# Optimization experiments

Hardware: AMD Instinct MI355X
Metric: run time of the kernel (lower is better)

## Reference

```python
import jax, jax.numpy as jnp
import numpy as np

BETA = 0.9      # LIF leak
THRESH = 1.0    # snntorch Leaky default threshold
SLOPE = 25.0    # fast_sigmoid surrogate slope

@jax.custom_vjp
def spike(x):
    # Heaviside forward, fast_sigmoid surrogate backward
    return (x > 0).astype(x.dtype)

def _spike_fwd(x):
    return spike(x), x

def _spike_bwd(x, g):
    return (g / (SLOPE * jnp.abs(x) + 1.0) ** 2,)

spike.defvjp(_spike_fwd, _spike_bwd)


def setup_inputs() -> dict:
    key = jax.random.key(0)
    k0, k1, k2, k3, k4 = jax.random.split(key, 5)
    B, T, I, H, C = 256, 100, 512, 1024, 8
    x = jax.random.normal(k0, (B, T, I), dtype=jnp.float32)
    s1 = 1.0 / np.sqrt(I)
    s2 = 1.0 / np.sqrt(H)
    W1 = jax.random.uniform(k1, (H, I), jnp.float32, -s1, s1)
    b1 = jax.random.uniform(k2, (H,), jnp.float32, -s1, s1)
    W2 = jax.random.uniform(k3, (C, H), jnp.float32, -s2, s2)
    b2 = jax.random.uniform(k4, (C,), jnp.float32, -s2, s2)
    return {"x": x, "W1": W1, "b1": b1, "W2": W2, "b2": b2}


def reference(x, W1, b1, W2, b2):
    # x: [B, T, I]
    B, T, I = x.shape
    H = W1.shape[0]
    # fc1 for all timesteps as one big GEMM (same math as per-step loop).
    cur = jnp.einsum('bti,hi->tbh', x, W1) + b1  # [T, B, H]

    def step(mem, c):
        # snntorch Leaky (reset_mechanism='subtract'):
        reset = spike(mem - THRESH)
        mem_new = BETA * mem + c - reset * THRESH
        spk = spike(mem_new - THRESH)
        return mem_new, spk

    mem0 = jnp.zeros((B, H), dtype=x.dtype)
    _, spk_rec = jax.lax.scan(step, mem0, cur)  # spk_rec: [T, B, H]

    # sum_t (spk_t @ W2.T + b2) == (sum_t spk_t) @ W2.T + T*b2
    spk_sum = spk_rec.sum(axis=0)  # [B, H]
    logits = spk_sum @ W2.T + T * b2  # [B, C]
    return logits
```

## Files before the change

kernel.cpp:

```cpp
#include <hip/hip_runtime.h>


#define B_   256
#define T_   100
#define I_   512
#define H_   1024
#define C_   8
#define M_   (B_ * T_)
#define SC   64.0f
#define ISC  (1.0f / 4096.0f)

#define CELL_  512
#define SHALF_ 16384
#define PANEL_ 32768

typedef _Float16 half8 __attribute__((ext_vector_type(8)));
typedef float floatx16 __attribute__((ext_vector_type(16)));

__device__ __forceinline__ void ld_g2l(const _Float16* g, _Float16* l) {
    __builtin_amdgcn_global_load_lds(
        (const __attribute__((address_space(1))) void*)g,
        (__attribute__((address_space(3))) void*)l, 16, 0, 0);
}

__global__ void __launch_bounds__(256)
split_all(const float* __restrict__ x, const float* __restrict__ W1,
          const float* __restrict__ b2, _Float16* __restrict__ Asp,
          float* __restrict__ out) {
    const int tid = threadIdx.x;
    const int lane = tid & 63;
    const int w = tid >> 6;
    const int p = blockIdx.x;
    int g = p * 256 + tid;
    if (g < B_ * C_) out[g] = 100.0f * b2[g & (C_ - 1)];

    const bool isA = (p < 800);
    const int pl = isA ? p : (p - 800);
    const float* srcm = isA ? x : W1;
    _Float16* dstp = Asp + (size_t)(isA ? pl : (800 + pl)) * PANEL_;
#pragma unroll 2
    for (int j = 0; j < 8; ++j) {
        const int rl = j * 4 + w;
        const int r  = pl * 32 + rl;
        const float* src = srcm + (size_t)r * I_ + lane * 8;
        float4 v0 = *(const float4*)(src);
        float4 v1 = *(const float4*)(src + 4);
        float vv[8] = {v0.x, v0.y, v0.z, v0.w, v1.x, v1.y, v1.z, v1.w};
        half8 hi, lo;
#pragma unroll
        for (int q = 0; q < 8; ++q) {
            float s = vv[q] * SC;
            _Float16 h = (_Float16)s;
            hi[q] = h;
            lo[q] = (_Float16)(s - (float)h);
        }
        _Float16* d = dstp + (lane >> 1) * CELL_ + rl * 16 + (lane & 1) * 8;
        *(half8*)(d) = hi;
        *(half8*)(d + SHALF_) = lo;
    }
}

#define MFMA32(A, Bv, Cacc) \
    Cacc = __builtin_amdgcn_mfma_f32_32x32x16_f16(A, Bv, Cacc, 0, 0, 0)

#define STAGE(dd, cc) do {                                           \
    _Float16* lb = &sm.buf[0][0] + (dd) * 12288;                     \
    ld_g2l(gah  + (cc) * CELL_, lb + w * 512);                       \
    ld_g2l(gal  + (cc) * CELL_, lb + 2048 + w * 512);                \
    ld_g2l(gbh0 + (cc) * CELL_, lb + 4096 + w * 1024);               \
    ld_g2l(gbh1 + (cc) * CELL_, lb + 4096 + w * 1024 + 512);         \
    ld_g2l(gbl0 + (cc) * CELL_, lb + 8192 + w * 1024);               \
    ld_g2l(gbl1 + (cc) * CELL_, lb + 8192 + w * 1024 + 512);         \
} while (0)

#define COMPUTE(dd) do {                                             \
    const _Float16* bb = &sm.buf[0][0] + (dd) * 12288;               \
    half8 ah[2], al[2], bh[4], bl[4];                                \
    _Pragma("unroll")                                                \
    for (int f = 0; f < 2; ++f) {                                    \
        ah[f] = *(const half8*)(bb + ra + f * 512);                  \
        al[f] = *(const half8*)(bb + 2048 + ra + f * 512);           \
    }                                                                \
    _Pragma("unroll")                                                \
    for (int f = 0; f < 4; ++f) {                                    \
        bh[f] = *(const half8*)(bb + 4096 + rb + f * 512);           \
        bl[f] = *(const half8*)(bb + 8192 + rb + f * 512);           \
    }                                                                \
    _Pragma("unroll")                                                \
    for (int fm = 0; fm < 2; ++fm) {                                 \
        _Pragma("unroll")                                            \
        for (int fn = 0; fn < 4; ++fn) {                             \
            MFMA32(ah[fm], bh[fn], acc[fm][fn]);                     \
            MFMA32(ah[fm], bl[fn], acc[fm][fn]);                     \
            MFMA32(al[fm], bh[fn], acc[fm][fn]);                     \
        }                                                            \
    }                                                                \
} while (0)

__global__ void __launch_bounds__(256, 2)
snn_mfma(const _Float16* __restrict__ Asp, const _Float16* __restrict__ Wsp,
         const float* __restrict__ b1, const float* __restrict__ W2,
         float* __restrict__ logits) {
    __shared__ union {
        __align__(16) _Float16 buf[2][12288];
        float Cs[32 * 256];
    } sm;
    const int tid = threadIdx.x;
    const int lane = tid & 63;
    const int w = tid >> 6;

    const int xcd = blockIdx.x & 7;
    const int jj = blockIdx.x >> 3;
    const int b  = xcd * 32 + (jj >> 2);
    const int n0 = (jj & 3) * 256;

    const int wm = (w >> 1) * 64;
    const int wn = (w & 1) * 128;
    const int l31 = lane & 31;
    const int q2 = lane >> 5;

    const int lp = lane ^ ((lane >> 3) & 7);
    const int ra_row = b * T_ + w * 32 + (lp >> 1);
    const int rb_row = n0 + w * 64 + (lp >> 1);
    const _Float16* gah = Asp + (size_t)(ra_row >> 5) * PANEL_
                              + (ra_row & 31) * 16 + (lp & 1) * 8;
    const _Float16* gal = gah + SHALF_;
    const _Float16* gbh0 = Wsp + (size_t)(rb_row >> 5) * PANEL_
                               + (rb_row & 31) * 16 + (lp & 1) * 8;
    const _Float16* gbh1 = gbh0 + PANEL_;
    const _Float16* gbl0 = gbh0 + SHALF_;
    const _Float16* gbl1 = gbh1 + SHALF_;

    const int swz = ((l31 >> 2) & 7) << 3;
    const int ra = ((wm + l31) * 16 + q2 * 8) ^ swz;
    const int rb = ((wn + l31) * 16 + q2 * 8) ^ swz;

    floatx16 acc[2][4];
#pragma unroll
    for (int i = 0; i < 2; ++i)
#pragma unroll
        for (int j = 0; j < 4; ++j)
#pragma unroll
            for (int e = 0; e < 16; ++e) acc[i][j][e] = 0.f;

    STAGE(0, 0);
#pragma unroll 2
    for (int c = 0; c < 31; ++c) {
        const int d = c & 1;
        STAGE(d ^ 1, c + 1);
        asm volatile("s_waitcnt vmcnt(6)" ::: "memory");
        __builtin_amdgcn_s_barrier();
        COMPUTE(d);
        __builtin_amdgcn_s_barrier();
        asm volatile("" ::: "memory");
    }
    asm volatile("s_waitcnt vmcnt(0)" ::: "memory");
    __builtin_amdgcn_s_barrier();
    COMPUTE(1);
    __syncthreads();

    float b1c[4];
#pragma unroll
    for (int fn = 0; fn < 4; ++fn) b1c[fn] = b1[n0 + wn + fn * 32 + l31];

    float mem = 0.f, ss = 0.f;

#pragma unroll
    for (int p = 0; p < 4; ++p) {
        const int fm = p & 1;
        if ((w >> 1) == (p >> 1)) {
#pragma unroll
            for (int r = 0; r < 16; ++r) {
                const int row = (r & 3) + 8 * (r >> 2) + 4 * q2;
                float* dst = &sm.Cs[row * 256 + wn + l31];
#pragma unroll
                for (int fn = 0; fn < 4; ++fn)
                    dst[fn * 32] = acc[fm][fn][r] * ISC + b1c[fn];
            }
        }
        __syncthreads();
        const int nt = (p == 3) ? 4 : 32;
#pragma unroll 8
        for (int t = 0; t < nt; ++t) {
            float cv = sm.Cs[t * 256 + tid];
            float reset = (mem > 1.0f) ? 1.0f : 0.0f;
            mem = 0.9f * mem + cv - reset;
            ss += (mem > 1.0f) ? 1.0f : 0.0f;
        }
        __syncthreads();
    }

#pragma unroll
    for (int cc = 0; cc < C_; ++cc) {
        float v = ss * W2[cc * H_ + n0 + tid];
#pragma unroll
        for (int off = 32; off; off >>= 1) v += __shfl_down(v, off, 64);
        if (lane == 0) atomicAdd(&logits[b * C_ + cc], v);
    }
}

extern "C" void kernel_launch(void* const* d_in, const int* in_sizes, int n_in,
                              void* d_out, int out_size, void* d_ws, size_t ws_size,
                              hipStream_t stream) {
    const float* x  = (const float*)d_in[0];
    const float* W1 = (const float*)d_in[1];
    const float* b1 = (const float*)d_in[2];
    const float* W2 = (const float*)d_in[3];
    const float* b2 = (const float*)d_in[4];
    float* out = (float*)d_out;

    char* ws = (char*)d_ws;
    _Float16* Asp = (_Float16*)ws;
    _Float16* Wsp = Asp + (size_t)800 * PANEL_;

    hipLaunchKernelGGL(split_all, dim3(832), dim3(256), 0, stream,
                       x, W1, b2, Asp, out);
    hipLaunchKernelGGL(snn_mfma, dim3(B_ * 4), dim3(256), 0, stream,
                       Asp, Wsp, b1, W2, out);
}
```

Before: 209.6 us.

## Triple-buffer LDS staging with split-phase MFMA and interleaved async loads

Replaces the double-buffered global-to-LDS pipeline with a three-stage ring buffer that prefetches two K-chunks ahead. Each iteration is split into two half-N phases, and the async loads for the next-but-one chunk are interleaved between them. MFMA blocks are wrapped in s_setprio, and one of the two barriers per iteration is dropped. LDS use rises from 48KB to 72KB per block, which may lower occupancy below the 2 blocks per CU the launch bounds request. The extra LDS reads of B fragments are spread across the two phases.

```diff
diff --git a/kernel.cpp b/kernel.cpp
--- a/kernel.cpp
+++ b/kernel.cpp
@@ -63,46 +63,12 @@
 #define MFMA32(A, Bv, Cacc) \
     Cacc = __builtin_amdgcn_mfma_f32_32x32x16_f16(A, Bv, Cacc, 0, 0, 0)
 
-#define STAGE(dd, cc) do {                                           \
-    _Float16* lb = &sm.buf[0][0] + (dd) * 12288;                     \
-    ld_g2l(gah  + (cc) * CELL_, lb + w * 512);                       \
-    ld_g2l(gal  + (cc) * CELL_, lb + 2048 + w * 512);                \
-    ld_g2l(gbh0 + (cc) * CELL_, lb + 4096 + w * 1024);               \
-    ld_g2l(gbh1 + (cc) * CELL_, lb + 4096 + w * 1024 + 512);         \
-    ld_g2l(gbl0 + (cc) * CELL_, lb + 8192 + w * 1024);               \
-    ld_g2l(gbl1 + (cc) * CELL_, lb + 8192 + w * 1024 + 512);         \
-} while (0)
-
-#define COMPUTE(dd) do {                                             \
-    const _Float16* bb = &sm.buf[0][0] + (dd) * 12288;               \
-    half8 ah[2], al[2], bh[4], bl[4];                                \
-    _Pragma("unroll")                                                \
-    for (int f = 0; f < 2; ++f) {                                    \
-        ah[f] = *(const half8*)(bb + ra + f * 512);                  \
-        al[f] = *(const half8*)(bb + 2048 + ra + f * 512);           \
-    }                                                                \
-    _Pragma("unroll")                                                \
-    for (int f = 0; f < 4; ++f) {                                    \
-        bh[f] = *(const half8*)(bb + 4096 + rb + f * 512);           \
-        bl[f] = *(const half8*)(bb + 8192 + rb + f * 512);           \
-    }                                                                \
-    _Pragma("unroll")                                                \
-    for (int fm = 0; fm < 2; ++fm) {                                 \
-        _Pragma("unroll")                                            \
-        for (int fn = 0; fn < 4; ++fn) {                             \
-            MFMA32(ah[fm], bh[fn], acc[fm][fn]);                     \
-            MFMA32(ah[fm], bl[fn], acc[fm][fn]);                     \
-            MFMA32(al[fm], bh[fn], acc[fm][fn]);                     \
-        }                                                            \
-    }                                                                \
-} while (0)
-
 __global__ void __launch_bounds__(256, 2)
 snn_mfma(const _Float16* __restrict__ Asp, const _Float16* __restrict__ Wsp,
          const float* __restrict__ b1, const float* __restrict__ W2,
          float* __restrict__ logits) {
     __shared__ union {
-        __align__(16) _Float16 buf[2][12288];
+        __align__(16) _Float16 buf[3][12288];
         float Cs[32 * 256];
     } sm;
     const int tid = threadIdx.x;
@@ -143,20 +109,75 @@
 #pragma unroll
             for (int e = 0; e < 16; ++e) acc[i][j][e] = 0.f;
 
-    STAGE(0, 0);
-#pragma unroll 2
-    for (int c = 0; c < 31; ++c) {
-        const int d = c & 1;
-        STAGE(d ^ 1, c + 1);
-        asm volatile("s_waitcnt vmcnt(6)" ::: "memory");
+#pragma unroll
+    for (int c0 = 0; c0 < 2; ++c0) {
+        _Float16* nb = &sm.buf[0][0] + c0 * 12288;
+        ld_g2l(gah  + c0 * CELL_, nb + w * 512);
+        ld_g2l(gal  + c0 * CELL_, nb + 2048 + w * 512);
+        ld_g2l(gbh0 + c0 * CELL_, nb + 4096 + w * 1024);
+        ld_g2l(gbh1 + c0 * CELL_, nb + 4096 + w * 1024 + 512);
+        ld_g2l(gbl0 + c0 * CELL_, nb + 8192 + w * 1024);
+        ld_g2l(gbl1 + c0 * CELL_, nb + 8192 + w * 1024 + 512);
+    }
+    asm volatile("s_waitcnt vmcnt(6)" ::: "memory");
+    __builtin_amdgcn_s_barrier();
+
+    int bufc = 0, bufn = 2;
+    for (int c = 0; c < 32; ++c) {
+        const _Float16* bb = &sm.buf[0][0] + bufc * 12288;
+        _Float16* nb = &sm.buf[0][0] + bufn * 12288;
+        half8 ah[2], al[2], bh[2], bl[2];
+        ah[0] = *(const half8*)(bb + ra);
+        ah[1] = *(const half8*)(bb + ra + 512);
+        al[0] = *(const half8*)(bb + 2048 + ra);
+        al[1] = *(const half8*)(bb + 2048 + ra + 512);
+        bh[0] = *(const half8*)(bb + 4096 + rb);
+        bh[1] = *(const half8*)(bb + 4096 + rb + 512);
+        bl[0] = *(const half8*)(bb + 8192 + rb);
+        bl[1] = *(const half8*)(bb + 8192 + rb + 512);
+        if (c < 30) {
+            const int cc = c + 2;
+            ld_g2l(gah  + cc * CELL_, nb + w * 512);
+            ld_g2l(gal  + cc * CELL_, nb + 2048 + w * 512);
+            ld_g2l(gbh0 + cc * CELL_, nb + 4096 + w * 1024);
+        }
+        __builtin_amdgcn_s_setprio(1);
+        MFMA32(ah[0], bh[0], acc[0][0]); MFMA32(ah[0], bh[1], acc[0][1]);
+        MFMA32(ah[1], bh[0], acc[1][0]); MFMA32(ah[1], bh[1], acc[1][1]);
+        MFMA32(ah[0], bl[0], acc[0][0]); MFMA32(ah[0], bl[1], acc[0][1]);
+        MFMA32(ah[1], bl[0], acc[1][0]); MFMA32(ah[1], bl[1], acc[1][1]);
+        MFMA32(al[0], bh[0], acc[0][0]); MFMA32(al[0], bh[1], acc[0][1]);
+        MFMA32(al[1], bh[0], acc[1][0]); MFMA32(al[1], bh[1], acc[1][1]);
+        __builtin_amdgcn_s_setprio(0);
         __builtin_amdgcn_s_barrier();
-        COMPUTE(d);
-        __builtin_amdgcn_s_barrier();
-        asm volatile("" ::: "memory");
-    }
-    asm volatile("s_waitcnt vmcnt(0)" ::: "memory");
-    __builtin_amdgcn_s_barrier();
-    COMPUTE(1);
+        bh[0] = *(const half8*)(bb + 4096 + rb + 1024);
+        bh[1] = *(const half8*)(bb + 4096 + rb + 1536);
+        bl[0] = *(const half8*)(bb + 8192 + rb + 1024);
+        bl[1] = *(const half8*)(bb + 8192 + rb + 1536);
+        if (c < 30) {
+            const int cc = c + 2;
+            ld_g2l(gbh1 + cc * CELL_, nb + 4096 + w * 1024 + 512);
+            ld_g2l(gbl0 + cc * CELL_, nb + 8192 + w * 1024);
+            ld_g2l(gbl1 + cc * CELL_, nb + 8192 + w * 1024 + 512);
+        }
+        __builtin_amdgcn_s_setprio(1);
+        MFMA32(ah[0], bh[0], acc[0][2]); MFMA32(ah[0], bh[1], acc[0][3]);
+        MFMA32(ah[1], bh[0], acc[1][2]); MFMA32(ah[1], bh[1], acc[1][3]);
+        MFMA32(ah[0], bl[0], acc[0][2]); MFMA32(ah[0], bl[1], acc[0][3]);
+        MFMA32(ah[1], bl[0], acc[1][2]); MFMA32(ah[1], bl[1], acc[1][3]);
+        MFMA32(al[0], bh[0], acc[0][2]); MFMA32(al[0], bh[1], acc[0][3]);
+        MFMA32(al[1], bh[0], acc[1][2]); MFMA32(al[1], bh[1], acc[1][3]);
+        __builtin_amdgcn_s_setprio(0);
+        if (c < 30) {
+            asm volatile("s_waitcnt vmcnt(6)" ::: "memory");
+            __builtin_amdgcn_s_barrier();
+        } else if (c == 30) {
+            asm volatile("s_waitcnt vmcnt(0)" ::: "memory");
+            __builtin_amdgcn_s_barrier();
+        }
+        bufc = (bufc == 2) ? 0 : bufc + 1;
+        bufn = (bufn == 2) ? 0 : bufn + 1;
+    }
     __syncthreads();
 
     float b1c[4];
```

After: 204.3 us. -2.5%, faster.
